# Performance work log

Measured on AMD Instinct MI355X. Metric: run time of the kernel, lower is better.

The kernel has to match this reference:

```python
import jax, jax.numpy as jnp
import numpy as np
from jax import lax

SCALE = (8.0, 8.0)
IGNORE_THRES = 0.5
BAD_CONF_WEIGHT = 1.25
NUM_CLASSES = 20
NB, NA, NH, NW = 16, 5, 128, 128
MAX_T = 50


def _inv_tanh(y):
    # matches inv_tanh: saturates to +/-2 outside (-1, 1)
    yc = jnp.clip(y, -1.0 + 1e-6, 1.0 - 1e-6)
    v = 0.5 * jnp.log((1.0 + yc) / (1.0 - yc))
    return jnp.where(y <= -1.0, -2.0, jnp.where(y >= 1.0, 2.0, v))


def _iou_xywh(b1, b2):
    # bbox_iou(..., x1y1x2y2=False): corners are center +/- w, center +/- h (full extents, faithful to source)
    b1x1, b1x2 = b1[0] - b1[2], b1[0] + b1[2]
    b1y1, b1y2 = b1[1] - b1[3], b1[1] + b1[3]
    b2x1, b2x2 = b2[0] - b2[2], b2[0] + b2[2]
    b2y1, b2y2 = b2[1] - b2[3], b2[1] + b2[3]
    iw = jnp.maximum(jnp.minimum(b1x2, b2x2) - jnp.maximum(b1x1, b2x1) + 1.0, 0.0)
    ih = jnp.maximum(jnp.minimum(b1y2, b2y2) - jnp.maximum(b1y1, b2y1) + 1.0, 0.0)
    inter = iw * ih
    a1 = (b1x2 - b1x1 + 1.0) * (b1y2 - b1y1 + 1.0)
    a2 = (b2x2 - b2x1 + 1.0) * (b2y2 - b2y1 + 1.0)
    return inter / (a1 + a2 - inter + 1e-16)


def build_targets(pred_boxes, pred_conf, pred_cls, target, target_sizes, anchors_s):
    nB, nA, nH, nW = pred_conf.shape
    T = target.shape[1]
    nC = pred_cls.shape[-1]
    f32 = jnp.float32
    init = (jnp.zeros((nB, nA, nH, nW), f32),      # mask
            jnp.ones((nB, nA, nH, nW), f32),       # conf_mask
            jnp.zeros((nB, nA, nH, nW), f32),      # tx
            jnp.zeros((nB, nA, nH, nW), f32),      # ty
            jnp.zeros((nB, nA, nH, nW), f32),      # tw
            jnp.zeros((nB, nA, nH, nW), f32),      # th
            jnp.zeros((nB, nA, nH, nW), f32),      # tconf
            jnp.zeros((nB, nA, nH, nW, nC), f32),  # tcls
            jnp.zeros((), f32),                    # nGT
            jnp.zeros((), f32))                    # nCorrect

    def step(state, i):
        mask, conf_mask, tx, ty, tw, th, tconf, tcls, nGT, nCorrect = state
        b, t = i // T, i % T
        row = target[b, t]
        gx, gy = row[0] / SCALE[0], row[1] / SCALE[1]
        gh, gw = row[3] / SCALE[1], row[4] / SCALE[0]
        valid = (t < target_sizes[b]) & (gw != 0.0) & (gh != 0.0)
        gi = jnp.clip(gx.astype(jnp.int32), 0, nW - 1)
        gj = jnp.clip(gy.astype(jnp.int32), 0, nH - 1)
        # anchor matching: IoU of corner boxes (0,0,w,h) with +1 convention
        inter = (jnp.maximum(jnp.minimum(gw, anchors_s[:, 0]) + 1.0, 0.0)
                 * jnp.maximum(jnp.minimum(gh, anchors_s[:, 1]) + 1.0, 0.0))
        anch_ious = inter / ((gw + 1.0) * (gh + 1.0)
                             + (anchors_s[:, 0] + 1.0) * (anchors_s[:, 1] + 1.0)
                             - inter + 1e-16)
        bn = jnp.argmax(anch_ious)
        # zero conf_mask at cell for anchors over ignore threshold, then set best anchor
        cm_cell = jnp.where(valid & (anch_ious > IGNORE_THRES), 0.0, conf_mask[b, :, gj, gi])
        conf_mask = conf_mask.at[b, :, gj, gi].set(cm_cell)

        def upd(arr, val):
            return arr.at[b, bn, gj, gi].set(jnp.where(valid, val, arr[b, bn, gj, gi]))

        mask = upd(mask, 1.0)
        conf_mask = upd(conf_mask, 1.0)
        tx = upd(tx, _inv_tanh(gx - (gi.astype(f32) + 0.5)))
        ty = upd(ty, _inv_tanh(gy - (gj.astype(f32) + 0.5)))
        tw = upd(tw, jnp.log(gw / anchors_s[bn, 0] + 1e-16))
        th = upd(th, jnp.log(gh / anchors_s[bn, 1] + 1e-16))
        tconf = upd(tconf, 1.0)
        cls_row = row[13:]
        tcls = tcls.at[b, bn, gj, gi].set(jnp.where(valid, cls_row, tcls[b, bn, gj, gi]))
        iou = _iou_xywh(jnp.stack([gx, gy, gw, gh]), pred_boxes[b, bn, gj, gi])
        correct = (valid & (iou > 0.5)
                   & (jnp.argmax(pred_cls[b, bn, gj, gi]) == jnp.argmax(cls_row))
                   & (pred_conf[b, bn, gj, gi] > 0.0))
        nGT = nGT + valid.astype(f32)
        nCorrect = nCorrect + correct.astype(f32)
        return (mask, conf_mask, tx, ty, tw, th, tconf, tcls, nGT, nCorrect), None

    state, _ = lax.scan(step, init, jnp.arange(nB * T))
    return state


def setup_inputs():
    key = jax.random.key(0)
    k1, k2, k3, k4, k5, k6, k7 = jax.random.split(key, 7)
    prediction = jax.random.normal(k1, (NB, NA, NH, NW, 6 + NUM_CLASSES), dtype=jnp.float32)
    xs = jax.random.uniform(k2, (NB, MAX_T)) * (NW * SCALE[0])
    ys = jax.random.uniform(k3, (NB, MAX_T)) * (NH * SCALE[1])
    hs = 8.0 + jax.random.uniform(k4, (NB, MAX_T)) * 192.0
    ws = 8.0 + jax.random.uniform(k5, (NB, MAX_T)) * 192.0
    cls_id = jax.random.randint(k6, (NB, MAX_T), 0, NUM_CLASSES)
    onehot = jax.nn.one_hot(cls_id, NUM_CLASSES, dtype=jnp.float32)
    target = jnp.zeros((NB, MAX_T, 13 + NUM_CLASSES), dtype=jnp.float32)
    target = target.at[..., 0].set(xs).at[..., 1].set(ys).at[..., 3].set(hs).at[..., 4].set(ws)
    target = target.at[..., 13:].set(onehot)
    target_sizes = jax.random.randint(k7, (NB,), 1, MAX_T + 1).astype(jnp.int32)
    anchors = jnp.array([[16., 16.], [32., 24.], [64., 48.], [128., 96.], [256., 128.]], dtype=jnp.float32)
    return {"prediction": prediction, "target": target, "target_sizes": target_sizes, "anchors": anchors}


def reference(prediction, target, target_sizes, anchors):
    nB, nA, nH, nW, _ = prediction.shape
    x, y = prediction[..., 1], prediction[..., 2]
    h, w = prediction[..., 4], prediction[..., 5]
    pred_conf = prediction[..., 0]
    pred_cls = prediction[..., 6:]
    anchors_s = anchors / jnp.array([SCALE[0], SCALE[1]], dtype=jnp.float32)
    grid_x = jnp.arange(nW, dtype=jnp.float32)[None, None, None, :]
    grid_y = jnp.arange(nH, dtype=jnp.float32)[None, None, :, None]
    aw = anchors_s[:, 0][None, :, None, None]
    ah = anchors_s[:, 1][None, :, None, None]
    pred_boxes = jnp.stack([jnp.tanh(x) + 0.5 + grid_x,
                            jnp.tanh(y) + 0.5 + grid_y,
                            jnp.exp(w) * aw,
                            jnp.exp(h) * ah], axis=-1)
    # build_targets operates on detached data (torch uses .cpu().data)
    mask, conf_mask, tx, ty, tw, th, tconf, tcls, nGT, nCorrect = build_targets(
        lax.stop_gradient(pred_boxes), lax.stop_gradient(pred_conf),
        lax.stop_gradient(pred_cls), lax.stop_gradient(target), target_sizes, anchors_s)
    m = mask
    cm_false = conf_mask * (1.0 - mask)
    nM = jnp.maximum(m.sum(), 1.0)
    nF = jnp.maximum(cm_false.sum(), 1.0)
    mmse = lambda p, t: jnp.sum(((p - t) ** 2) * m) / nM  # masked-mean MSE
    loss_x = mmse(x, tx)
    loss_y = mmse(y, ty)
    loss_w = mmse(w, tw)
    loss_h = mmse(h, th)
    bce = lambda logit, z: jax.nn.softplus(logit) - logit * z  # BCE-with-logits
    loss_conf = (BAD_CONF_WEIGHT * jnp.sum(bce(pred_conf, tconf) * cm_false) / nF
                 + jnp.sum(bce(pred_conf, tconf) * m) / nM)
    logp = jax.nn.log_softmax(pred_cls, axis=-1)
    tlabel = jnp.argmax(tcls, axis=-1)
    ce = -jnp.take_along_axis(logp, tlabel[..., None], axis=-1)[..., 0]
    loss_cls = (1.0 / nB) * jnp.sum(ce * m) / nM
    loss = loss_x + loss_y + loss_w + loss_h + loss_conf + loss_cls
    nProposals = jnp.sum(pred_conf > 0.0).astype(jnp.float32)
    recall = jnp.where(nGT > 0, nCorrect / jnp.maximum(nGT, 1.0), 1.0)
    precision = jnp.where(nProposals > 0, nCorrect / jnp.maximum(nProposals, 1.0), 1.0)
    return loss, recall, precision
```

## Files before the change

### kernel.cpp

```cpp
#include <hip/hip_runtime.h>
#include <math.h>

#define kNB 16
#define kNA 5
#define kNH 128
#define kNW 128
#define kMaxT 50
#define kNC 20
#define kCH 26
#define kRowW 33
#define kNTot (kNB*kNA*kNH*kNW)
#define DENSE_BLOCKS 2048
#define kStride (DENSE_BLOCKS * 256)
#define TOT_F4 (kNTot * kCH / 4)
#define SP_BASE (2 * DENSE_BLOCKS)
#define SP_N 11


__device__ __forceinline__ float softplus_fast(float x) {
    return fmaxf(x, 0.0f) + __logf(1.0f + __expf(-fabsf(x)));
}
__device__ __forceinline__ float softplusf(float x) {
    return fmaxf(x, 0.0f) + log1pf(expf(-fabsf(x)));
}

__device__ __forceinline__ double wave_sum(double v) {
    #pragma unroll
    for (int off = 32; off > 0; off >>= 1) v += __shfl_down(v, off, 64);
    return v;
}

__device__ __forceinline__ float inv_tanhf(float y) {
    float yc = fminf(fmaxf(y, -1.0f + 1e-6f), 1.0f - 1e-6f);
    float v = 0.5f * logf((1.0f + yc) / (1.0f - yc));
    return (y <= -1.0f) ? -2.0f : ((y >= 1.0f) ? 2.0f : v);
}

__device__ __forceinline__ void conf_step(const float4 v, int r, float& sp, int& prop) {
    bool is0 = (r == 0);
    bool has = is0 | (r == 24);
    float p = is0 ? v.x : v.z;
    float s = softplus_fast(p);
    sp += has ? s : 0.0f;
    prop += (has & (p > 0.0f)) ? 1 : 0;
}

extern "C" __global__ __launch_bounds__(256)
void yolo_main(const float* __restrict__ pred, const float* __restrict__ target,
               const int* __restrict__ tsizes, const float* __restrict__ anchors,
               double* __restrict__ ws)
{
    const int tid = threadIdx.x;

    if (blockIdx.x >= kNB) {
        __shared__ double s_red[8];
        const int bid = (int)blockIdx.x - kNB;
        const float4* __restrict__ p4 = (const float4*)pred;
        const int t0 = bid * 256 + tid;
        const int r0 = (4 * t0) % 26;
        float sp = 0.0f;
        int prop = 0;

        constexpr int OFF[17] = {0,18,10,2,20,12,4,22,14,6,24,16,8,0,18,10,2};

        #pragma unroll
        for (int g = 0; g < 2; ++g) {
            const int base = t0 + (8 * g) * kStride;
            float4 v[8];
            #pragma unroll
            for (int j = 0; j < 8; ++j) v[j] = p4[base + j * kStride];
            #pragma unroll
            for (int j = 0; j < 8; ++j) {
                int rk = r0 + OFF[8 * g + j];
                rk = (rk >= 26) ? rk - 26 : rk;
                conf_step(v[j], rk, sp, prop);
            }
        }
        {
            const int idx = t0 + 16 * kStride;
            if (idx < TOT_F4) {
                int rt = r0 + OFF[16];
                rt = (rt >= 26) ? rt - 26 : rt;
                conf_step(p4[idx], rt, sp, prop);
            }
        }

        double spd = wave_sum((double)sp);
        double prd = wave_sum((double)prop);
        int wid = tid >> 6;
        if ((tid & 63) == 0) { s_red[wid] = spd; s_red[4 + wid] = prd; }
        __syncthreads();
        if (tid == 0) {
            ws[bid]                = s_red[0] + s_red[1] + s_red[2] + s_red[3];
            ws[DENSE_BLOCKS + bid] = s_red[4] + s_red[5] + s_red[6] + s_red[7];
        }
        return;
    }

    const int b = blockIdx.x;
    __shared__ float s_t[kMaxT][kRowW];
    __shared__ float s_aw[kNA], s_ah[kNA];
    __shared__ int s_cell[kMaxT], s_bn[kMaxT], s_zm[kMaxT], s_valid[kMaxT];
    __shared__ int s_label[kMaxT];
    __shared__ float s_tx[kMaxT], s_ty[kMaxT], s_tw[kMaxT], s_th[kMaxT];

    for (int i = tid; i < kMaxT * kRowW; i += 256)
        ((float*)s_t)[i] = target[(long long)b * kMaxT * kRowW + i];
    if (tid < kNA) {
        s_aw[tid] = anchors[tid * 2 + 0] / 8.0f;
        s_ah[tid] = anchors[tid * 2 + 1] / 8.0f;
    }
    __syncthreads();

    const int tsz = tsizes[b];
    double ngt = 0.0, ncorr = 0.0;
    int myCell = -1;

    if (tid < kMaxT) {
        const float* row = s_t[tid];
        float gx = row[0] / 8.0f, gy = row[1] / 8.0f;
        float gh = row[3] / 8.0f, gw = row[4] / 8.0f;
        int valid = (tid < tsz) && (gw != 0.0f) && (gh != 0.0f);
        int gi = min(max((int)gx, 0), kNW - 1);
        int gj = min(max((int)gy, 0), kNH - 1);

        float best = -1.0f; int bn = 0; int zm = 0;
        #pragma unroll
        for (int a = 0; a < kNA; ++a) {
            float aw = s_aw[a], ah = s_ah[a];
            float inter = fmaxf(fminf(gw, aw) + 1.0f, 0.0f) * fmaxf(fminf(gh, ah) + 1.0f, 0.0f);
            float iou = inter / ((gw + 1.0f) * (gh + 1.0f) + (aw + 1.0f) * (ah + 1.0f) - inter + 1e-16f);
            if (iou > best) { best = iou; bn = a; }
            if (iou > 0.5f) zm |= (1 << a);
        }

        int lab = 0; float lbest = row[13];
        #pragma unroll
        for (int c = 1; c < kNC; ++c)
            if (row[13 + c] > lbest) { lbest = row[13 + c]; lab = c; }

        long long base = ((((long long)b * kNA + bn) * kNH + gj) * kNW + gi) * kCH;
        float pc = pred[base + 0];
        float px = tanhf(pred[base + 1]) + 0.5f + (float)gi;
        float py = tanhf(pred[base + 2]) + 0.5f + (float)gj;
        float ph = expf(pred[base + 4]) * s_ah[bn];
        float pw = expf(pred[base + 5]) * s_aw[bn];
        float b1x1 = gx - gw, b1x2 = gx + gw, b1y1 = gy - gh, b1y2 = gy + gh;
        float b2x1 = px - pw, b2x2 = px + pw, b2y1 = py - ph, b2y2 = py + ph;
        float iw = fmaxf(fminf(b1x2, b2x2) - fmaxf(b1x1, b2x1) + 1.0f, 0.0f);
        float ih = fmaxf(fminf(b1y2, b2y2) - fmaxf(b1y1, b2y1) + 1.0f, 0.0f);
        float inter2 = iw * ih;
        float a1 = (b1x2 - b1x1 + 1.0f) * (b1y2 - b1y1 + 1.0f);
        float a2 = (b2x2 - b2x1 + 1.0f) * (b2y2 - b2y1 + 1.0f);
        float iou2 = inter2 / (a1 + a2 - inter2 + 1e-16f);
        int plab = 0; float pbest = pred[base + 6];
        #pragma unroll
        for (int c = 1; c < kNC; ++c) {
            float v = pred[base + 6 + c];
            if (v > pbest) { pbest = v; plab = c; }
        }
        int correct = valid && (iou2 > 0.5f) && (plab == lab) && (pc > 0.0f);

        myCell = gj * kNW + gi;
        s_cell[tid] = myCell; s_bn[tid] = bn; s_zm[tid] = zm; s_valid[tid] = valid;
        s_label[tid] = lab;
        s_tx[tid] = inv_tanhf(gx - ((float)gi + 0.5f));
        s_ty[tid] = inv_tanhf(gy - ((float)gj + 0.5f));
        s_tw[tid] = logf(gw / s_aw[bn] + 1e-16f);
        s_th[tid] = logf(gh / s_ah[bn] + 1e-16f);
        ngt = (double)valid; ncorr = (double)correct;
    }
    __syncthreads();

    double S_excl = 0, cnt_excl = 0, nM = 0, bce = 0;
    double sx = 0, sy = 0, sw_ = 0, sh_ = 0, ce = 0;

    if (tid < kMaxT) {
        int lastTouch[kNA], lastSet[kNA], lastCm[kNA];
        #pragma unroll
        for (int a = 0; a < kNA; ++a) { lastTouch[a] = -1; lastSet[a] = -1; lastCm[a] = 0; }

        for (int tp = 0; tp < kMaxT; ++tp) {
            if (!s_valid[tp] || s_cell[tp] != myCell) continue;
            int bnp = s_bn[tp], zmp = s_zm[tp];
            #pragma unroll
            for (int a = 0; a < kNA; ++a) {
                bool setr = (bnp == a);
                if (setr || ((zmp >> a) & 1)) { lastTouch[a] = tp; lastCm[a] = setr ? 1 : 0; }
                if (setr) lastSet[a] = tp;
            }
        }

        int gj = myCell >> 7, gi = myCell & 127;
        #pragma unroll
        for (int a = 0; a < kNA; ++a) {
            if (lastTouch[a] != tid) continue;
            bool msk = lastSet[a] >= 0;
            bool cmf = lastCm[a] != 0;
            if (!msk && cmf) continue;
            long long base = ((((long long)b * kNA + a) * kNH + gj) * kNW + gi) * kCH;
            float pc = pred[base];
            float sp2 = softplusf(pc);
            S_excl += (double)sp2; cnt_excl += 1.0;
            if (msk) {
                int ts = lastSet[a];
                nM += 1.0; bce += (double)(sp2 - pc);
                float dx = pred[base + 1] - s_tx[ts];
                float dy = pred[base + 2] - s_ty[ts];
                float dh = pred[base + 4] - s_th[ts];
                float dw = pred[base + 5] - s_tw[ts];
                sx += (double)(dx * dx); sy += (double)(dy * dy);
                sw_ += (double)(dw * dw); sh_ += (double)(dh * dh);
                float m20 = pred[base + 6];
                #pragma unroll
                for (int c = 1; c < kNC; ++c) m20 = fmaxf(m20, pred[base + 6 + c]);
                float es = 0.0f;
                #pragma unroll
                for (int c = 0; c < kNC; ++c) es += expf(pred[base + 6 + c] - m20);
                ce += (double)(m20 + logf(es) - pred[base + 6 + s_label[ts]]);
            }
        }
    }

    if (tid < 64) {
        S_excl = wave_sum(S_excl); cnt_excl = wave_sum(cnt_excl);
        nM = wave_sum(nM); bce = wave_sum(bce);
        sx = wave_sum(sx); sy = wave_sum(sy); sw_ = wave_sum(sw_); sh_ = wave_sum(sh_);
        ce = wave_sum(ce); ngt = wave_sum(ngt); ncorr = wave_sum(ncorr);
        if (tid == 0) {
            double* o = &ws[SP_BASE + b * SP_N];
            o[0] = S_excl; o[1] = cnt_excl; o[2] = nM; o[3] = bce;
            o[4] = sx; o[5] = sy; o[6] = sw_; o[7] = sh_;
            o[8] = ce; o[9] = ngt; o[10] = ncorr;
        }
    }
}

extern "C" __global__ __launch_bounds__(256)
void yolo_finalize(const double* __restrict__ ws, float* __restrict__ out) {
    __shared__ double s_red[8];
    __shared__ double s_sp[kNB * SP_N];
    __shared__ double s_acc[SP_N];
    const int tid = threadIdx.x;

    if (tid < kNB * SP_N) s_sp[tid] = ws[SP_BASE + tid];

    double sp = 0.0, pr = 0.0;
    for (int i = tid; i < DENSE_BLOCKS; i += 256) {
        sp += ws[i];
        pr += ws[DENSE_BLOCKS + i];
    }
    sp = wave_sum(sp); pr = wave_sum(pr);
    int wid = tid >> 6;
    if ((tid & 63) == 0) { s_red[wid] = sp; s_red[4 + wid] = pr; }
    __syncthreads();

    if (tid < SP_N) {
        double acc = 0.0;
        #pragma unroll
        for (int b = 0; b < kNB; ++b) acc += s_sp[b * SP_N + tid];
        s_acc[tid] = acc;
    }
    __syncthreads();

    if (tid == 0) {
        double S_all = s_red[0] + s_red[1] + s_red[2] + s_red[3];
        double nProp = s_red[4] + s_red[5] + s_red[6] + s_red[7];
        double S_excl = s_acc[0], cnt_excl = s_acc[1];
        double nMc = s_acc[2], bce = s_acc[3];
        double sx = s_acc[4], sy = s_acc[5], sw = s_acc[6], sh = s_acc[7];
        double ce = s_acc[8], nGT = s_acc[9], nCorr = s_acc[10];
        double nM = fmax(nMc, 1.0);
        double nF = fmax((double)kNTot - cnt_excl, 1.0);
        double loss_conf = 1.25 * (S_all - S_excl) / nF + bce / nM;
        double loss = (sx + sy + sw + sh) / nM + loss_conf + (ce / nM) / 16.0;
        double recall = (nGT > 0.0) ? nCorr / fmax(nGT, 1.0) : 1.0;
        double precision = (nProp > 0.0) ? nCorr / fmax(nProp, 1.0) : 1.0;
        out[0] = (float)loss;
        out[1] = (float)recall;
        out[2] = (float)precision;
    }
}

extern "C" void kernel_launch(void* const* d_in, const int* in_sizes, int n_in,
                              void* d_out, int out_size, void* d_ws, size_t ws_size,
                              hipStream_t stream) {
    const float* pred    = (const float*)d_in[0];
    const float* target  = (const float*)d_in[1];
    const int*   tsizes  = (const int*)d_in[2];
    const float* anchors = (const float*)d_in[3];
    float* out = (float*)d_out;
    double* ws = (double*)d_ws;

    yolo_main<<<DENSE_BLOCKS + kNB, 256, 0, stream>>>(pred, target, tsizes, anchors, ws);
    yolo_finalize<<<1, 256, 0, stream>>>(ws, out);
}
```

Measured before the change: 48.69 us.

## Gather only confidence channel per cell instead of streaming full prediction tensor

The confidence softplus/proposal reduction now loads just the float4 containing each cell's confidence value, computed from the cell index, rather than streaming every float4 of the prediction tensor and masking by channel position. Block count is reduced so each thread handles four cells. This cuts the bytes the reduction pulls from memory, at the cost of strided, less coalesced loads.

```diff
diff --git a/kernel.cpp b/kernel.cpp
--- a/kernel.cpp
+++ b/kernel.cpp
@@ -10,9 +10,8 @@
 #define kCH 26
 #define kRowW 33
 #define kNTot (kNB*kNA*kNH*kNW)
-#define DENSE_BLOCKS 2048
-#define kStride (DENSE_BLOCKS * 256)
-#define TOT_F4 (kNTot * kCH / 4)
+#define DENSE_BLOCKS 1280
+#define kTS (DENSE_BLOCKS * 256)
 #define SP_BASE (2 * DENSE_BLOCKS)
 #define SP_N 11
 
@@ -34,15 +33,6 @@
     float yc = fminf(fmaxf(y, -1.0f + 1e-6f), 1.0f - 1e-6f);
     float v = 0.5f * logf((1.0f + yc) / (1.0f - yc));
     return (y <= -1.0f) ? -2.0f : ((y >= 1.0f) ? 2.0f : v);
-}
-
-__device__ __forceinline__ void conf_step(const float4 v, int r, float& sp, int& prop) {
-    bool is0 = (r == 0);
-    bool has = is0 | (r == 24);
-    float p = is0 ? v.x : v.z;
-    float s = softplus_fast(p);
-    sp += has ? s : 0.0f;
-    prop += (has & (p > 0.0f)) ? 1 : 0;
 }
 
 extern "C" __global__ __launch_bounds__(256)
@@ -57,33 +47,21 @@
         const int bid = (int)blockIdx.x - kNB;
         const float4* __restrict__ p4 = (const float4*)pred;
         const int t0 = bid * 256 + tid;
-        const int r0 = (4 * t0) % 26;
-        float sp = 0.0f;
-        int prop = 0;
-
-        constexpr int OFF[17] = {0,18,10,2,20,12,4,22,14,6,24,16,8,0,18,10,2};
-
-        #pragma unroll
-        for (int g = 0; g < 2; ++g) {
-            const int base = t0 + (8 * g) * kStride;
-            float4 v[8];
-            #pragma unroll
-            for (int j = 0; j < 8; ++j) v[j] = p4[base + j * kStride];
-            #pragma unroll
-            for (int j = 0; j < 8; ++j) {
-                int rk = r0 + OFF[8 * g + j];
-                rk = (rk >= 26) ? rk - 26 : rk;
-                conf_step(v[j], rk, sp, prop);
-            }
-        }
-        {
-            const int idx = t0 + 16 * kStride;
-            if (idx < TOT_F4) {
-                int rt = r0 + OFF[16];
-                rt = (rt >= 26) ? rt - 26 : rt;
-                conf_step(p4[idx], rt, sp, prop);
-            }
-        }
+        const bool odd = (t0 & 1);
+
+        float4 v0 = p4[(13 * (t0 + 0 * kTS)) >> 1];
+        float4 v1 = p4[(13 * (t0 + 1 * kTS)) >> 1];
+        float4 v2 = p4[(13 * (t0 + 2 * kTS)) >> 1];
+        float4 v3 = p4[(13 * (t0 + 3 * kTS)) >> 1];
+
+        float p0 = odd ? v0.z : v0.x;
+        float p1 = odd ? v1.z : v1.x;
+        float p2 = odd ? v2.z : v2.x;
+        float p3 = odd ? v3.z : v3.x;
+
+        float sp = softplus_fast(p0) + softplus_fast(p1)
+                 + softplus_fast(p2) + softplus_fast(p3);
+        int prop = (p0 > 0.0f) + (p1 > 0.0f) + (p2 > 0.0f) + (p3 > 0.0f);
 
         double spd = wave_sum((double)sp);
         double prd = wave_sum((double)prop);
```

Result: no change. 49.21 us (+1.1%).
